# Kernel tuning notes

Hardware: AMD Instinct MI355X
Metric: run time of the kernel (lower is better)

## Reference

```python
import jax, jax.numpy as jnp
import numpy as np

B, N, H = 8, 1024, 32


def _mlp(x, W1, b1, W2, b2, W3, b3):
    # Normalization(mean=0, std=1) is identity; leaky_relu slope 0.01 (torch default)
    h = jax.nn.leaky_relu(x @ W1 + b1)
    h = jax.nn.leaky_relu(h @ W2 + b2)
    return jnp.tanh(h @ W3 + b3)


def setup_inputs() -> dict:
    key = jax.random.key(0)
    ks = jax.random.split(key, 10)
    s = 0.1  # small init scale for numerical sanity under tanh
    return {
        "x": jax.random.normal(ks[0], (B, N, 2), dtype=jnp.float32),
        "A": jax.random.uniform(ks[1], (N, N), dtype=jnp.float32),
        "Wm1": jax.random.normal(ks[2], (2, H), dtype=jnp.float32) * s,
        "bm1": jnp.zeros((H,), jnp.float32),
        "Wm2": jax.random.normal(ks[3], (H, H), dtype=jnp.float32) * s,
        "bm2": jnp.zeros((H,), jnp.float32),
        "Wm3": jax.random.normal(ks[4], (H, 1), dtype=jnp.float32) * s,
        "bm3": jnp.zeros((1,), jnp.float32),
        "Wx1": jax.random.normal(ks[5], (2, H), dtype=jnp.float32) * s,
        "bx1": jnp.zeros((H,), jnp.float32),
        "Wx2": jax.random.normal(ks[6], (H, H), dtype=jnp.float32) * s,
        "bx2": jnp.zeros((H,), jnp.float32),
        "Wx3": jax.random.normal(ks[7], (H, 1), dtype=jnp.float32) * s,
        "bx3": jnp.zeros((1,), jnp.float32),
    }


def reference(x, A, Wm1, bm1, Wm2, bm2, Wm3, bm3, Wx1, bx1, Wx2, bx2, Wx3, bx3):
    rho = x[:, :, 0]  # [B, N]
    V = x[:, :, 1]    # [B, N]
    # pairwise message: message[b, i, j] = (rho[b,i]+rho[b,j], V[b,i]+V[b,j])
    msg = jnp.stack(
        [rho[:, None, :] + rho[:, :, None], V[:, None, :] + V[:, :, None]],
        axis=-1,
    )  # [B, N, N, 2]
    me = _mlp(msg, Wm1, bm1, Wm2, bm2, Wm3, bm3)[..., 0]  # [B, N, N]
    msg_sum = jnp.einsum("bij,ij->bi", me, A)  # adjacency-weighted sum over j
    x2 = jnp.stack([rho, msg_sum], axis=-1)  # [B, N, 2]
    return _mlp(x2, Wx1, bx1, Wx2, bx2, Wx3, bx3)  # [B, N, 1]
```

## Files before the change

### kernel.cpp

```cpp
#include <hip/hip_runtime.h>

#define NB 8
#define NN 1024
#define NH 32

#define FP 99
#define CW 6.0f
#define RW 7.5f
#define UW (CW * RW / (CW + RW))

__device__ __forceinline__ float leaky(float x) { return fmaxf(x, 0.01f * x); }

__device__ __forceinline__ float fast_tanh(float x) {
    float e = __builtin_amdgcn_exp2f(x * 2.88539008177792681f);
    return 1.0f - 2.0f * __builtin_amdgcn_rcpf(1.0f + e);
}

#define SWZ_ADD(v, imm) \
    v += __int_as_float(__builtin_amdgcn_ds_swizzle(__float_as_int(v), imm))

__device__ __forceinline__ unsigned bf16r(float f) {
    unsigned u = __float_as_uint(f);
    return (u + 0x7FFFu + ((u >> 16) & 1u)) >> 16;
}

__global__ __launch_bounds__(256) void eval_kernel(
    const float* __restrict__ Wm1, const float* __restrict__ bm1,
    const float* __restrict__ Wm2, const float* __restrict__ bm2,
    const float* __restrict__ Wm3, const float* __restrict__ bm3,
    float* __restrict__ tabf) {
    __shared__ __align__(16) float sW2[1024];
    __shared__ float sW1[64], sb1[32], sb2[32], sW3[32];
    __shared__ float sb3;
    const int tid = threadIdx.x;
#pragma unroll
    for (int q = 0; q < 4; ++q) sW2[tid + 256 * q] = Wm2[tid + 256 * q];
    if (tid < 64) sW1[tid] = Wm1[tid];
    if (tid < 32) { sb1[tid] = bm1[tid]; sb2[tid] = bm2[tid]; sW3[tid] = Wm3[tid]; }
    if (tid == 0) sb3 = bm3[0];
    __syncthreads();

    const int gid = blockIdx.x * 256 + tid;
    if (gid >= FP * FP) return;
    const int iy = gid / FP;
    const int ix = gid - iy * FP;

    const float hu = 2.0f * UW / (float)(FP - 1);
    const float us = fmaf((float)ix, hu, -UW);
    const float ut = fmaf((float)iy, hu, -UW);
    const float s = us / (1.0f - fabsf(us) / CW);
    const float t = ut / (1.0f - fabsf(ut) / CW);

    float h1[NH];
#pragma unroll
    for (int k = 0; k < NH; ++k)
        h1[k] = leaky(s * sW1[k] + t * sW1[32 + k] + sb1[k]);

    float acc[NH];
#pragma unroll
    for (int h = 0; h < NH; ++h) acc[h] = sb2[h];
#pragma unroll
    for (int k = 0; k < NH; ++k) {
#pragma unroll
        for (int h4 = 0; h4 < 8; ++h4) {
            const float4 wv = *(const float4*)(sW2 + k * 32 + h4 * 4);
            acc[h4 * 4 + 0] = fmaf(h1[k], wv.x, acc[h4 * 4 + 0]);
            acc[h4 * 4 + 1] = fmaf(h1[k], wv.y, acc[h4 * 4 + 1]);
            acc[h4 * 4 + 2] = fmaf(h1[k], wv.z, acc[h4 * 4 + 2]);
            acc[h4 * 4 + 3] = fmaf(h1[k], wv.w, acc[h4 * 4 + 3]);
        }
    }
    float z = sb3;
#pragma unroll
    for (int h = 0; h < NH; ++h) z = fmaf(leaky(acc[h]), sW3[h], z);
    tabf[gid] = fast_tanh(z);
}

__global__ __launch_bounds__(256) void assemble_kernel(
    const float* __restrict__ tabf, uint2* __restrict__ tq) {
    const int gid = blockIdx.x * 256 + threadIdx.x;
    if (gid >= FP * FP) return;
    const int iy = gid / FP;
    const int ix = gid - iy * FP;
    if (ix >= FP - 1 || iy >= FP - 1) { tq[gid] = make_uint2(0u, 0u); return; }
    const float f00 = tabf[gid];
    const float f10 = tabf[gid + 1];
    const float f01 = tabf[gid + FP];
    uint2 cell;
    cell.x = __float_as_uint(f00);
    cell.y = bf16r(f10 - f00) | (bf16r(f01 - f00) << 16);
    tq[gid] = cell;
}

__global__ __launch_bounds__(1024, 8) void edge_out_kernel(
    const float* __restrict__ x, const float* __restrict__ A,
    const uint2* __restrict__ tq,
    const float* __restrict__ Wx1, const float* __restrict__ bx1,
    const float* __restrict__ Wx2, const float* __restrict__ bx2,
    const float* __restrict__ Wx3, const float* __restrict__ bx3,
    float* __restrict__ out) {
    __shared__ uint2 sfq[FP * FP];

    const int tid = threadIdx.x;
    {
        const float4* __restrict__ src = (const float4*)tq;
        float4* dst = (float4*)sfq;
        for (int idx = tid; idx < (FP * FP) / 2; idx += 1024) dst[idx] = src[idx];
        if (tid == 0) sfq[FP * FP - 1] = tq[FP * FP - 1];
    }
    __syncthreads();

    const int wave = tid >> 6;
    const int lane = tid & 63;
    const int w    = blockIdx.x * 16 + wave;
    const int i    = w >> 3;
    const int b    = w & 7;
    const int node = b * NN + i;

    const float2 xi = ((const float2*)x)[node];
    const float4* __restrict__ xb4 = (const float4*)((const float2*)x + b * NN);
    const float2* __restrict__ Ar2 = (const float2*)(A + (size_t)i * NN);

    const float hu     = 2.0f * UW / (float)(FP - 1);
    const float inv_hu = 1.0f / hu;
    const float fhi    = (float)(FP - 1) - 0.001f;
    const float rcw    = 1.0f / CW;

    float ms0 = 0.0f, ms1 = 0.0f, ms2 = 0.0f, ms3 = 0.0f;
#pragma unroll
    for (int g = 0; g < 2; ++g) {
        float4 xv[4]; float2 av[4];
#pragma unroll
        for (int q = 0; q < 4; ++q) {
            const int p = (g * 4 + q) * 64 + lane;
            xv[q] = xb4[p];
            av[q] = Ar2[p];
        }
        int   idxq[8];
        float asq[8], atq[8];
#pragma unroll
        for (int q = 0; q < 4; ++q) {
#pragma unroll
            for (int e = 0; e < 2; ++e) {
                const float s = xi.x + (e ? xv[q].z : xv[q].x);
                const float t = xi.y + (e ? xv[q].w : xv[q].y);
                const float us = s * __builtin_amdgcn_rcpf(fmaf(fabsf(s), rcw, 1.0f));
                const float ut = t * __builtin_amdgcn_rcpf(fmaf(fabsf(t), rcw, 1.0f));
                const float fs = fminf(fmaxf((us + UW) * inv_hu, 0.0f), fhi);
                const float ft = fminf(fmaxf((ut + UW) * inv_hu, 0.0f), fhi);
                const float fsf = floorf(fs), ftf = floorf(ft);
                asq[q * 2 + e] = fs - fsf;
                atq[q * 2 + e] = ft - ftf;
                idxq[q * 2 + e] = (int)ftf * FP + (int)fsf;
            }
        }
        uint2 cqv[8];
#pragma unroll
        for (int q = 0; q < 8; ++q) cqv[q] = sfq[idxq[q]];
#pragma unroll
        for (int q = 0; q < 8; ++q) {
            const float c00 = __uint_as_float(cqv[q].x);
            const float dcs = __uint_as_float(cqv[q].y << 16);
            const float dct = __uint_as_float(cqv[q].y & 0xFFFF0000u);
            const float me  = fmaf(atq[q], dct, fmaf(asq[q], dcs, c00));
            const float aw  = (q & 1) ? av[q >> 1].y : av[q >> 1].x;
            if      ((q & 3) == 0) ms0 = fmaf(me, aw, ms0);
            else if ((q & 3) == 1) ms1 = fmaf(me, aw, ms1);
            else if ((q & 3) == 2) ms2 = fmaf(me, aw, ms2);
            else                   ms3 = fmaf(me, aw, ms3);
        }
    }
    float msum = (ms0 + ms1) + (ms2 + ms3);

    SWZ_ADD(msum, 0x041F);
    SWZ_ADD(msum, 0x081F);
    SWZ_ADD(msum, 0x101F);
    SWZ_ADD(msum, 0x201F);
    SWZ_ADD(msum, 0x401F);
    msum += __shfl_xor(msum, 32, 64);

    const float rho = xi.x;
    const int h = lane & 31;
    float acc = bx2[h];
#pragma unroll
    for (int k = 0; k < NH; ++k) {
        const float h1k = leaky(fmaf(msum, Wx1[32 + k], fmaf(rho, Wx1[k], bx1[k])));
        acc = fmaf(h1k, Wx2[k * 32 + h], acc);
    }
    float sv = (lane < 32) ? leaky(acc) * Wx3[h] : 0.0f;
    SWZ_ADD(sv, 0x041F);
    SWZ_ADD(sv, 0x081F);
    SWZ_ADD(sv, 0x101F);
    SWZ_ADD(sv, 0x201F);
    SWZ_ADD(sv, 0x401F);
    sv += __shfl_xor(sv, 32, 64);
    if (lane == 0) out[node] = fast_tanh(sv + bx3[0]);
}

extern "C" void kernel_launch(void* const* d_in, const int* in_sizes, int n_in,
                              void* d_out, int out_size, void* d_ws, size_t ws_size,
                              hipStream_t stream) {
    const float* x   = (const float*)d_in[0];
    const float* A   = (const float*)d_in[1];
    const float* Wm1 = (const float*)d_in[2];
    const float* bm1 = (const float*)d_in[3];
    const float* Wm2 = (const float*)d_in[4];
    const float* bm2 = (const float*)d_in[5];
    const float* Wm3 = (const float*)d_in[6];
    const float* bm3 = (const float*)d_in[7];
    const float* Wx1 = (const float*)d_in[8];
    const float* bx1 = (const float*)d_in[9];
    const float* Wx2 = (const float*)d_in[10];
    const float* bx2 = (const float*)d_in[11];
    const float* Wx3 = (const float*)d_in[12];
    const float* bx3 = (const float*)d_in[13];

    uint2* tq   = (uint2*)d_ws;
    float* tabf = (float*)(tq + FP * FP);
    float* out  = (float*)d_out;

    const int nblk = (FP * FP + 255) / 256;
    eval_kernel<<<dim3(nblk), dim3(256), 0, stream>>>(
        Wm1, bm1, Wm2, bm2, Wm3, bm3, tabf);
    assemble_kernel<<<dim3(nblk), dim3(256), 0, stream>>>(tabf, tq);
    edge_out_kernel<<<dim3(NB * NN / 16), dim3(1024), 0, stream>>>(
        x, A, tq, Wx1, bx1, Wx2, bx2, Wx3, bx3, out);
}
```

Baseline: 103.6 us.

## Fuse table assembly into edge kernel and spread table MLP over lanes

The separate assemble kernel is removed. Each edge_out block now builds the packed bf16-delta interpolation cells itself, straight from the float table, while filling shared memory. The table-evaluation kernel now assigns 32 lanes per grid point, one hidden unit each, and reduces with ds_swizzle instead of running the full 32x32 MLP per thread. This removes one launch and the intermediate table buffer and gives the small eval stage far more parallelism. The cost is that every edge block repeats the assembly work: integer divides and three global loads per cell.

```diff
diff --git a/kernel.cpp b/kernel.cpp
--- a/kernel.cpp
+++ b/kernel.cpp
@@ -29,21 +29,16 @@
     const float* __restrict__ Wm2, const float* __restrict__ bm2,
     const float* __restrict__ Wm3, const float* __restrict__ bm3,
     float* __restrict__ tabf) {
-    __shared__ __align__(16) float sW2[1024];
-    __shared__ float sW1[64], sb1[32], sb2[32], sW3[32];
-    __shared__ float sb3;
-    const int tid = threadIdx.x;
-#pragma unroll
-    for (int q = 0; q < 4; ++q) sW2[tid + 256 * q] = Wm2[tid + 256 * q];
-    if (tid < 64) sW1[tid] = Wm1[tid];
-    if (tid < 32) { sb1[tid] = bm1[tid]; sb2[tid] = bm2[tid]; sW3[tid] = Wm3[tid]; }
-    if (tid == 0) sb3 = bm3[0];
-    __syncthreads();
-
-    const int gid = blockIdx.x * 256 + tid;
-    if (gid >= FP * FP) return;
-    const int iy = gid / FP;
-    const int ix = gid - iy * FP;
+    const int tid  = threadIdx.x;
+    const int wav  = blockIdx.x * 4 + (tid >> 6);
+    const int lane = tid & 63;
+    const int half = lane >> 5;
+    const int h    = lane & 31;
+    const int p    = wav * 2 + half;
+    const bool valid = p < FP * FP;
+    const int pp = valid ? p : 0;
+    const int iy = pp / FP;
+    const int ix = pp - iy * FP;
 
     const float hu = 2.0f * UW / (float)(FP - 1);
     const float us = fmaf((float)ix, hu, -UW);
@@ -51,50 +46,24 @@
     const float s = us / (1.0f - fabsf(us) / CW);
     const float t = ut / (1.0f - fabsf(ut) / CW);
 
-    float h1[NH];
-#pragma unroll
-    for (int k = 0; k < NH; ++k)
-        h1[k] = leaky(s * sW1[k] + t * sW1[32 + k] + sb1[k]);
-
-    float acc[NH];
-#pragma unroll
-    for (int h = 0; h < NH; ++h) acc[h] = sb2[h];
+    float acc = bm2[h];
 #pragma unroll
     for (int k = 0; k < NH; ++k) {
-#pragma unroll
-        for (int h4 = 0; h4 < 8; ++h4) {
-            const float4 wv = *(const float4*)(sW2 + k * 32 + h4 * 4);
-            acc[h4 * 4 + 0] = fmaf(h1[k], wv.x, acc[h4 * 4 + 0]);
-            acc[h4 * 4 + 1] = fmaf(h1[k], wv.y, acc[h4 * 4 + 1]);
-            acc[h4 * 4 + 2] = fmaf(h1[k], wv.z, acc[h4 * 4 + 2]);
-            acc[h4 * 4 + 3] = fmaf(h1[k], wv.w, acc[h4 * 4 + 3]);
-        }
-    }
-    float z = sb3;
-#pragma unroll
-    for (int h = 0; h < NH; ++h) z = fmaf(leaky(acc[h]), sW3[h], z);
-    tabf[gid] = fast_tanh(z);
-}
-
-__global__ __launch_bounds__(256) void assemble_kernel(
-    const float* __restrict__ tabf, uint2* __restrict__ tq) {
-    const int gid = blockIdx.x * 256 + threadIdx.x;
-    if (gid >= FP * FP) return;
-    const int iy = gid / FP;
-    const int ix = gid - iy * FP;
-    if (ix >= FP - 1 || iy >= FP - 1) { tq[gid] = make_uint2(0u, 0u); return; }
-    const float f00 = tabf[gid];
-    const float f10 = tabf[gid + 1];
-    const float f01 = tabf[gid + FP];
-    uint2 cell;
-    cell.x = __float_as_uint(f00);
-    cell.y = bf16r(f10 - f00) | (bf16r(f01 - f00) << 16);
-    tq[gid] = cell;
+        const float h1k = leaky(s * Wm1[k] + t * Wm1[32 + k] + bm1[k]);
+        acc = fmaf(h1k, Wm2[k * 32 + h], acc);
+    }
+    float v = leaky(acc) * Wm3[h];
+    SWZ_ADD(v, 0x041F);
+    SWZ_ADD(v, 0x081F);
+    SWZ_ADD(v, 0x101F);
+    SWZ_ADD(v, 0x201F);
+    SWZ_ADD(v, 0x401F);
+    if (valid && h == 0) tabf[p] = fast_tanh(v + bm3[0]);
 }
 
 __global__ __launch_bounds__(1024, 8) void edge_out_kernel(
     const float* __restrict__ x, const float* __restrict__ A,
-    const uint2* __restrict__ tq,
+    const float* __restrict__ tabf,
     const float* __restrict__ Wx1, const float* __restrict__ bx1,
     const float* __restrict__ Wx2, const float* __restrict__ bx2,
     const float* __restrict__ Wx3, const float* __restrict__ bx3,
@@ -102,11 +71,16 @@
     __shared__ uint2 sfq[FP * FP];
 
     const int tid = threadIdx.x;
-    {
-        const float4* __restrict__ src = (const float4*)tq;
-        float4* dst = (float4*)sfq;
-        for (int idx = tid; idx < (FP * FP) / 2; idx += 1024) dst[idx] = src[idx];
-        if (tid == 0) sfq[FP * FP - 1] = tq[FP * FP - 1];
+    for (int gid = tid; gid < FP * FP; gid += 1024) {
+        const int giy = gid / FP;
+        const int gix = gid - giy * FP;
+        const float f00 = tabf[gid];
+        const float f10 = tabf[(gix < FP - 1) ? gid + 1 : gid];
+        const float f01 = tabf[(giy < FP - 1) ? gid + FP : gid];
+        uint2 cell;
+        cell.x = __float_as_uint(f00);
+        cell.y = bf16r(f10 - f00) | (bf16r(f01 - f00) << 16);
+        sfq[gid] = cell;
     }
     __syncthreads();
 
@@ -215,14 +189,13 @@
     const float* Wx3 = (const float*)d_in[12];
     const float* bx3 = (const float*)d_in[13];
 
-    uint2* tq   = (uint2*)d_ws;
-    float* tabf = (float*)(tq + FP * FP);
+    float* tabf = (float*)d_ws;
     float* out  = (float*)d_out;
 
-    const int nblk = (FP * FP + 255) / 256;
+    const int npairs = (FP * FP + 1) / 2;
+    const int nblk   = (npairs + 3) / 4;
     eval_kernel<<<dim3(nblk), dim3(256), 0, stream>>>(
         Wm1, bm1, Wm2, bm2, Wm3, bm3, tabf);
-    assemble_kernel<<<dim3(nblk), dim3(256), 0, stream>>>(tabf, tq);
     edge_out_kernel<<<dim3(NB * NN / 16), dim3(1024), 0, stream>>>(
-        x, A, tq, Wx1, bx1, Wx2, bx2, Wx3, bx3, out);
-}
+        x, A, tabf, Wx1, bx1, Wx2, bx2, Wx3, bx3, out);
+}
```

Result: faster. 95.16 us (-8.1%).
